# Performance work log

Hardware: AMD Instinct MI355X
Metric: run time of the kernel (lower is better)

Reference implementation:

```python
import jax, jax.numpy as jnp
import numpy as np

N, E, C_IN, C_OUT, K = 50000, 800000, 64, 64, 3

def setup_inputs() -> dict:
    key = jax.random.key(0)
    k1, k2, k3, k4, k5, k6 = jax.random.split(key, 6)
    x = jax.random.normal(k1, (N, C_IN), dtype=jnp.float32)
    row = jax.random.randint(k2, (E,), 0, N)
    col = jax.random.randint(k3, (E,), 0, N)
    # PyG ChebConv removes self loops; avoid generating them
    col = jnp.where(col == row, (col + 1) % N, col)
    edge_index = jnp.stack([row, col])
    edge_weight = jax.random.uniform(k4, (E,), dtype=jnp.float32)
    # ChebConv learned params: one [C_in, C_out] matrix per Chebyshev order, plus bias
    W = jax.random.normal(k5, (K, C_IN, C_OUT), dtype=jnp.float32) / np.sqrt(C_IN).astype(np.float32)
    b = jax.random.normal(k6, (C_OUT,), dtype=jnp.float32) * 0.01
    return {"x": x, "edge_index": edge_index, "edge_weight": edge_weight, "W": W, "b": b}


def reference(x, edge_index, edge_weight, W, b):
    row, col = edge_index[0], edge_index[1]
    # PyG ChebConv.__norm__ with sym normalization and lambda_max = 2.0:
    # L_hat = (2/lambda_max) * (I - D^{-1/2} A D^{-1/2}) - I = -D^{-1/2} A D^{-1/2}
    deg = jax.ops.segment_sum(edge_weight, row, num_segments=N)
    dis = jnp.where(deg > 0, jax.lax.rsqrt(deg), 0.0)  # deg_inv_sqrt, inf -> 0
    w = -dis[row] * edge_weight * dis[col]             # [E] normalized Laplacian weights

    def prop(h):  # sparse matvec: L_hat @ h, [N, C]
        return jax.ops.segment_sum(w[:, None] * h[col], row, num_segments=N)

    # Chebyshev recurrence: T0 = x, T1 = L_hat x, Tk = 2 L_hat T_{k-1} - T_{k-2}
    Tx0 = x
    out = Tx0 @ W[0]
    Tx1 = prop(Tx0)
    out = out + Tx1 @ W[1]
    for k in range(2, K):
        Tx2 = 2.0 * prop(Tx1) - Tx0
        out = out + Tx2 @ W[k]
        Tx0, Tx1 = Tx1, Tx2
    return jax.nn.relu(out + b)
```

## Files before the change

### kernel.cpp

```cpp
#include <hip/hip_runtime.h>
#include <hip/hip_bf16.h>

#define C 64

typedef unsigned short u16;
typedef unsigned int u32;
typedef unsigned long long u64;

__device__ __forceinline__ u16 f2bf_rne(float v) {
    unsigned u = __float_as_uint(v);
    u += 0x7FFFu + ((u >> 16) & 1u);
    return (u16)(u >> 16);
}
__device__ __forceinline__ float bf2f(u16 u) {
    return __uint_as_float((unsigned)u << 16);
}


__global__ __launch_bounds__(256) void p1hist_kernel(const int* __restrict__ row,
                                                     u32* __restrict__ hoff,
                                                     const float* __restrict__ x,
                                                     u16* __restrict__ xh,
                                                     int E, int NB, int total4, int nthreads) {
    __shared__ u32 h[256];
    int t = threadIdx.x;
    int b = blockIdx.x;
    h[t] = 0;
    __syncthreads();
    int base = b * 1024;
#pragma unroll
    for (int u = 0; u < 4; u++) {
        int e = base + u * 256 + t;
        if (e < E) {
            int r = row[e];
            atomicAdd(&h[r >> 8], 1u);
        }
    }
    __syncthreads();
    hoff[(size_t)b * 256 + t] = h[t];

    int gtid = b * 256 + t;
    for (int i = gtid; i < total4; i += nthreads) {
        float4 v = *(const float4*)(x + (size_t)i * 4);
        ushort4 o;
        o.x = f2bf_rne(v.x); o.y = f2bf_rne(v.y);
        o.z = f2bf_rne(v.z); o.w = f2bf_rne(v.w);
        *(ushort4*)(xh + (size_t)i * 4) = o;
    }
}

__global__ __launch_bounds__(256) void scanA_kernel(u32* __restrict__ hoff,
                                                    u32* __restrict__ T, int NB) {
    __shared__ u32 s[256];
    int t = threadIdx.x;
    int d = blockIdx.x;
    u32 carry = 0;
    int nchunk = (NB + 255) / 256;
    for (int ch = 0; ch < nchunk; ch++) {
        int idx = ch * 256 + t;
        u32 v = (idx < NB) ? hoff[(size_t)idx * 256 + d] : 0;
        s[t] = v;
        __syncthreads();
        for (int off = 1; off < 256; off <<= 1) {
            u32 u = (t >= off) ? s[t - off] : 0;
            __syncthreads();
            s[t] += u;
            __syncthreads();
        }
        if (idx < NB) hoff[(size_t)idx * 256 + d] = carry + s[t] - v;
        u32 tot = s[255];
        __syncthreads();
        carry += tot;
    }
    if (t == 0) T[d] = carry;
}

__global__ __launch_bounds__(256) void scanB_kernel(const u32* __restrict__ T,
                                                    u32* __restrict__ Tpre,
                                                    int* __restrict__ rowptr, int N) {
    __shared__ u32 s[256];
    int t = threadIdx.x;
    u32 v = T[t];
    s[t] = v;
    __syncthreads();
    for (int off = 1; off < 256; off <<= 1) {
        u32 u = (t >= off) ? s[t - off] : 0;
        __syncthreads();
        s[t] += u;
        __syncthreads();
    }
    Tpre[t] = s[t] - v;
    if (t == 255) {
        Tpre[256] = s[255];
        rowptr[N] = (int)s[255];
    }
}

__global__ __launch_bounds__(256) void p1scatter_kernel(const int* __restrict__ row,
                                                        const int* __restrict__ col,
                                                        const float* __restrict__ ew,
                                                        const u32* __restrict__ hoff,
                                                        const u32* __restrict__ Tpre,
                                                        u64* __restrict__ pay,
                                                        int E) {
    __shared__ u32 cur[256];
    int t = threadIdx.x;
    int b = blockIdx.x;
    cur[t] = Tpre[t] + hoff[(size_t)b * 256 + t];
    __syncthreads();
    int base = b * 1024;
#pragma unroll
    for (int u = 0; u < 4; u++) {
        int e = base + u * 256 + t;
        if (e < E) {
            u32 r = (u32)row[e];
            u32 c = (u32)col[e];
            u32 rc = (r << 16) | c;
            u32 pos = atomicAdd(&cur[r >> 8], 1u);
            pay[pos] = ((u64)rc << 32) | (u64)__float_as_uint(ew[e]);
        }
    }
}

__global__ __launch_bounds__(256) void p2_kernel(const u64* __restrict__ pay,
                                                 const u32* __restrict__ Tpre,
                                                 int* __restrict__ rowptr,
                                                 float* __restrict__ dis,
                                                 float2* __restrict__ ewc,
                                                 int N) {
    __shared__ u32 h[256];
    __shared__ u32 s[256];
    __shared__ u32 cur[256];
    __shared__ float dsum[256];
    int t = threadIdx.x;
    int bk = blockIdx.x;
    u32 base = Tpre[bk];
    u32 cnt = Tpre[bk + 1] - base;

    h[t] = 0;
    dsum[t] = 0.0f;
    __syncthreads();
    for (u32 j = t; j < cnt; j += 256) {
        u64 v = pay[base + j];
        u32 lr = (u32)(v >> 48) & 255u;
        atomicAdd(&h[lr], 1u);
    }
    __syncthreads();
    u32 hv = h[t];
    s[t] = hv;
    __syncthreads();
    for (int off = 1; off < 256; off <<= 1) {
        u32 u = (t >= off) ? s[t - off] : 0;
        __syncthreads();
        s[t] += u;
        __syncthreads();
    }
    u32 p = s[t] - hv;
    int r = bk * 256 + t;
    if (r < N) rowptr[r] = (int)(base + p);
    cur[t] = base + p;
    __syncthreads();
    for (u32 j = t; j < cnt; j += 256) {
        u64 v = pay[base + j];
        u32 rc = (u32)(v >> 32);
        u32 lr = (rc >> 16) & 255u;
        float w = __uint_as_float((u32)v);
        u32 pos = atomicAdd(&cur[lr], 1u);
        ewc[pos] = make_float2(w, __uint_as_float(rc & 0xffffu));
        atomicAdd(&dsum[lr], w);
    }
    __syncthreads();
    if (r < N) {
        float dv = dsum[t];
        dis[r] = (dv > 0.0f) ? rsqrtf(dv) : 0.0f;
    }
}

template <int NORM>
__global__ __launch_bounds__(256) void spmm2_kernel(
        const int* __restrict__ rowptr,
        float2* __restrict__ ewc,
        const float* __restrict__ dis,
        const u64* __restrict__ h64,
        float* __restrict__ out32,
        u64* __restrict__ outbf,
        int N) {
    __shared__ float2 eds[8][32];

    int tid  = threadIdx.x;
    int hw   = tid >> 5;
    int l32  = tid & 31;
    int e2   = l32 >> 4;
    int cq   = l32 & 15;

    int row = blockIdx.x * 8 + hw;
    if (row >= N) return;

    int beg = rowptr[row];
    int end = rowptr[row + 1];
    float disr = NORM ? dis[row] : 0.0f;

    float a0 = 0.f, a1 = 0.f, a2 = 0.f, a3 = 0.f;

    for (int base = beg; base < end; base += 32) {
        int idx = base + l32;
        bool valid = idx < end;
        float2 ed = valid ? ewc[idx] : make_float2(0.0f, __uint_as_float(0));
        if (NORM) {
            u32 c = __float_as_uint(ed.y);
            float w = -disr * ed.x * dis[c];
            ed = make_float2(w, __uint_as_float(c));
            if (valid) ewc[idx] = ed;
        }
        eds[hw][l32] = ed;
        int cnt = end - base; if (cnt > 32) cnt = 32;
        for (int j = 0; j < cnt; j += 4) {
            float2 f0 = eds[hw][j + e2];
            float2 f1 = eds[hw][j + 2 + e2];
            u32 c0 = __float_as_uint(f0.y);
            u32 c1 = __float_as_uint(f1.y);
            u64 hv0 = h64[(size_t)c0 * 16 + cq];
            u64 hv1 = h64[(size_t)c1 * 16 + cq];
            float w0 = f0.x, w1 = f1.x;
            u32 lo0 = (u32)hv0, hi0 = (u32)(hv0 >> 32);
            u32 lo1 = (u32)hv1, hi1 = (u32)(hv1 >> 32);
            a0 = fmaf(w0, bf2f((u16)(lo0 & 0xffffu)), a0);
            a1 = fmaf(w0, bf2f((u16)(lo0 >> 16)),     a1);
            a2 = fmaf(w0, bf2f((u16)(hi0 & 0xffffu)), a2);
            a3 = fmaf(w0, bf2f((u16)(hi0 >> 16)),     a3);
            a0 = fmaf(w1, bf2f((u16)(lo1 & 0xffffu)), a0);
            a1 = fmaf(w1, bf2f((u16)(lo1 >> 16)),     a1);
            a2 = fmaf(w1, bf2f((u16)(hi1 & 0xffffu)), a2);
            a3 = fmaf(w1, bf2f((u16)(hi1 >> 16)),     a3);
        }
    }

    a0 += __shfl_xor(a0, 16);
    a1 += __shfl_xor(a1, 16);
    a2 += __shfl_xor(a2, 16);
    a3 += __shfl_xor(a3, 16);

    if (e2 == 0) {
        float4 o = make_float4(a0, a1, a2, a3);
        *(float4*)(out32 + (size_t)row * C + 4 * cq) = o;
        u32 p0 = (u32)f2bf_rne(a0) | ((u32)f2bf_rne(a1) << 16);
        u32 p1 = (u32)f2bf_rne(a2) | ((u32)f2bf_rne(a3) << 16);
        outbf[(size_t)row * 16 + cq] = (u64)p0 | ((u64)p1 << 32);
    }
}

__global__ __launch_bounds__(256) void final_gemm_kernel(
        const float* __restrict__ x,
        const float* __restrict__ T1,
        const float* __restrict__ P,
        const float* __restrict__ W,
        const float* __restrict__ b,
        float* __restrict__ out, int N) {
    __shared__ float As[16][64];
    __shared__ float Ws[16][64];

    int t  = threadIdx.x;
    int tx = t & 15;
    int ty = t >> 4;
    int n0 = blockIdx.x * 64;

    int sn = t >> 2;
    int skb = (t & 3) * 4;

    float acc[4][4];
#pragma unroll
    for (int i = 0; i < 4; i++)
#pragma unroll
        for (int j = 0; j < 4; j++) acc[i][j] = 0.0f;

#pragma unroll 1
    for (int s = 0; s < 12; s++) {
        float4 wv = *(const float4*)(W + s * 1024 + t * 4);
        int nn = n0 + sn;
        float4 av = make_float4(0.f, 0.f, 0.f, 0.f);
        if (nn < N) {
            if (s < 4) {
                av = *(const float4*)(x + (size_t)nn * C + s * 16 + skb);
            } else if (s < 8) {
                av = *(const float4*)(T1 + (size_t)nn * C + (s - 4) * 16 + skb);
            } else {
                float4 pv = *(const float4*)(P + (size_t)nn * C + (s - 8) * 16 + skb);
                float4 xv = *(const float4*)(x + (size_t)nn * C + (s - 8) * 16 + skb);
                av = make_float4(2.0f * pv.x - xv.x, 2.0f * pv.y - xv.y,
                                 2.0f * pv.z - xv.z, 2.0f * pv.w - xv.w);
            }
        }
        __syncthreads();
        {
            int wk = (t * 4) >> 6;
            int wc = (t * 4) & 63;
            *(float4*)&Ws[wk][wc] = wv;
        }
        As[skb + 0][sn] = av.x;
        As[skb + 1][sn] = av.y;
        As[skb + 2][sn] = av.z;
        As[skb + 3][sn] = av.w;
        __syncthreads();

#pragma unroll
        for (int kk = 0; kk < 16; kk++) {
            float4 a4 = *(const float4*)&As[kk][ty * 4];
            float4 w4 = *(const float4*)&Ws[kk][tx * 4];
            float ar[4] = {a4.x, a4.y, a4.z, a4.w};
            float wr[4] = {w4.x, w4.y, w4.z, w4.w};
#pragma unroll
            for (int i = 0; i < 4; i++)
#pragma unroll
                for (int j = 0; j < 4; j++)
                    acc[i][j] = fmaf(ar[i], wr[j], acc[i][j]);
        }
    }

    float4 bv = *(const float4*)(b + tx * 4);
    float br[4] = {bv.x, bv.y, bv.z, bv.w};
#pragma unroll
    for (int i = 0; i < 4; i++) {
        int node = n0 + ty * 4 + i;
        if (node < N) {
            float4 o;
            o.x = fmaxf(acc[i][0] + br[0], 0.0f);
            o.y = fmaxf(acc[i][1] + br[1], 0.0f);
            o.z = fmaxf(acc[i][2] + br[2], 0.0f);
            o.w = fmaxf(acc[i][3] + br[3], 0.0f);
            *(float4*)(out + (size_t)node * C + tx * 4) = o;
        }
    }
}

extern "C" void kernel_launch(void* const* d_in, const int* in_sizes, int n_in,
                              void* d_out, int out_size, void* d_ws, size_t ws_size,
                              hipStream_t stream) {
    const float* x  = (const float*)d_in[0];
    const int*   ei = (const int*)d_in[1];
    const float* ew = (const float*)d_in[2];
    const float* W  = (const float*)d_in[3];
    const float* b  = (const float*)d_in[4];
    float* out = (float*)d_out;

    const int N = in_sizes[0] / C;
    const int E = in_sizes[2];
    const int* row = ei;
    const int* col = ei + E;

    char* ws = (char*)d_ws;
    size_t off = 0;
    auto alloc = [&](size_t bytes) {
        void* p = ws + off;
        off = (off + bytes + 255) & ~(size_t)255;
        return p;
    };
    const int NB = (E + 1023) / 1024;
    const int NBUCK = (N + 255) / 256;

    float*  dis    = (float*)alloc((size_t)N * 4);
    int*    rowptr = (int*)alloc((size_t)(N + 1) * 4);
    float2* ewc    = (float2*)alloc((size_t)E * 8);
    u64*    pay    = (u64*)alloc((size_t)E * 8);
    float*  T1     = (float*)alloc((size_t)N * C * 4);
    float*  P      = (float*)alloc((size_t)N * C * 4);
    u32*    hoff   = (u32*)alloc((size_t)NB * 256 * 4);
    u32*    T      = (u32*)alloc((size_t)256 * 4);
    u32*    Tpre   = (u32*)alloc((size_t)257 * 4);
    u16*    xh     = (u16*)alloc((size_t)N * C * 2);
    u16*    T1h    = (u16*)alloc((size_t)N * C * 2);
    u16*    Ph     = (u16*)alloc((size_t)N * C * 2);

    const int B = 256;
    int total4 = N * C / 4;

    p1hist_kernel<<<NB, B, 0, stream>>>(row, hoff, x, xh, E, NB, total4, NB * B);
    scanA_kernel<<<256, B, 0, stream>>>(hoff, T, NB);
    scanB_kernel<<<1, B, 0, stream>>>(T, Tpre, rowptr, N);
    p1scatter_kernel<<<NB, B, 0, stream>>>(row, col, ew, hoff, Tpre, pay, E);
    p2_kernel<<<NBUCK, B, 0, stream>>>(pay, Tpre, rowptr, dis, ewc, N);

    int spmm_blocks = (N + 7) / 8;
    spmm2_kernel<1><<<spmm_blocks, B, 0, stream>>>(rowptr, ewc, dis, (const u64*)xh,
                                                   T1, (u64*)T1h, N);
    spmm2_kernel<0><<<spmm_blocks, B, 0, stream>>>(rowptr, ewc, dis, (const u64*)T1h,
                                                   P, (u64*)Ph, N);

    final_gemm_kernel<<<(N + 63) / 64, B, 0, stream>>>(x, T1, P, W, b, out, N);
}
```

Baseline: 177.1 us.

## Fuse second SpMM into final GEMM, merge scan kernels, recompute edge norms

```diff
diff --git a/kernel.cpp b/kernel.cpp
--- a/kernel.cpp
+++ b/kernel.cpp
@@ -21,10 +21,12 @@
                                                      u32* __restrict__ hoff,
                                                      const float* __restrict__ x,
                                                      u16* __restrict__ xh,
+                                                     u32* __restrict__ done,
                                                      int E, int NB, int total4, int nthreads) {
     __shared__ u32 h[256];
     int t = threadIdx.x;
     int b = blockIdx.x;
+    if (b == 0 && t == 0) *done = 0;
     h[t] = 0;
     __syncthreads();
     int base = b * 1024;
@@ -49,9 +51,14 @@
     }
 }
 
-__global__ __launch_bounds__(256) void scanA_kernel(u32* __restrict__ hoff,
-                                                    u32* __restrict__ T, int NB) {
+__global__ __launch_bounds__(256) void scanAB_kernel(u32* __restrict__ hoff,
+                                                     u32* __restrict__ T,
+                                                     u32* __restrict__ Tpre,
+                                                     int* __restrict__ rowptr,
+                                                     u32* __restrict__ done,
+                                                     int N, int NB) {
     __shared__ u32 s[256];
+    __shared__ u32 lastFlag;
     int t = threadIdx.x;
     int d = blockIdx.x;
     u32 carry = 0;
@@ -73,26 +80,28 @@
         carry += tot;
     }
     if (t == 0) T[d] = carry;
-}
-
-__global__ __launch_bounds__(256) void scanB_kernel(const u32* __restrict__ T,
-                                                    u32* __restrict__ Tpre,
-                                                    int* __restrict__ rowptr, int N) {
-    __shared__ u32 s[256];
-    int t = threadIdx.x;
-    u32 v = T[t];
-    s[t] = v;
-    __syncthreads();
-    for (int off = 1; off < 256; off <<= 1) {
-        u32 u = (t >= off) ? s[t - off] : 0;
-        __syncthreads();
-        s[t] += u;
-        __syncthreads();
-    }
-    Tpre[t] = s[t] - v;
-    if (t == 255) {
-        Tpre[256] = s[255];
-        rowptr[N] = (int)s[255];
+    __threadfence();
+    if (t == 0) {
+        u32 tk = atomicAdd(done, 1u);
+        lastFlag = (tk == 255u) ? 1u : 0u;
+    }
+    __syncthreads();
+    if (lastFlag) {
+        __threadfence();
+        u32 v = T[t];
+        s[t] = v;
+        __syncthreads();
+        for (int off = 1; off < 256; off <<= 1) {
+            u32 u = (t >= off) ? s[t - off] : 0;
+            __syncthreads();
+            s[t] += u;
+            __syncthreads();
+        }
+        Tpre[t] = s[t] - v;
+        if (t == 255) {
+            Tpre[256] = s[255];
+            rowptr[N] = (int)s[255];
+        }
     }
 }
 
@@ -176,10 +185,9 @@
     }
 }
 
-template <int NORM>
-__global__ __launch_bounds__(256) void spmm2_kernel(
+__global__ __launch_bounds__(256) void spmm_t1_kernel(
         const int* __restrict__ rowptr,
-        float2* __restrict__ ewc,
+        const float2* __restrict__ ewc,
         const float* __restrict__ dis,
         const u64* __restrict__ h64,
         float* __restrict__ out32,
@@ -198,7 +206,7 @@
 
     int beg = rowptr[row];
     int end = rowptr[row + 1];
-    float disr = NORM ? dis[row] : 0.0f;
+    float disr = dis[row];
 
     float a0 = 0.f, a1 = 0.f, a2 = 0.f, a3 = 0.f;
 
@@ -206,32 +214,42 @@
         int idx = base + l32;
         bool valid = idx < end;
         float2 ed = valid ? ewc[idx] : make_float2(0.0f, __uint_as_float(0));
-        if (NORM) {
-            u32 c = __float_as_uint(ed.y);
-            float w = -disr * ed.x * dis[c];
-            ed = make_float2(w, __uint_as_float(c));
-            if (valid) ewc[idx] = ed;
-        }
-        eds[hw][l32] = ed;
+        u32 c = __float_as_uint(ed.y);
+        float wv = -disr * ed.x * dis[c];
+        eds[hw][l32] = make_float2(wv, ed.y);
         int cnt = end - base; if (cnt > 32) cnt = 32;
-        for (int j = 0; j < cnt; j += 4) {
+        int cnt8 = (cnt + 7) & ~7;
+        for (int j = 0; j < cnt8; j += 8) {
             float2 f0 = eds[hw][j + e2];
             float2 f1 = eds[hw][j + 2 + e2];
-            u32 c0 = __float_as_uint(f0.y);
-            u32 c1 = __float_as_uint(f1.y);
-            u64 hv0 = h64[(size_t)c0 * 16 + cq];
-            u64 hv1 = h64[(size_t)c1 * 16 + cq];
-            float w0 = f0.x, w1 = f1.x;
-            u32 lo0 = (u32)hv0, hi0 = (u32)(hv0 >> 32);
-            u32 lo1 = (u32)hv1, hi1 = (u32)(hv1 >> 32);
-            a0 = fmaf(w0, bf2f((u16)(lo0 & 0xffffu)), a0);
-            a1 = fmaf(w0, bf2f((u16)(lo0 >> 16)),     a1);
-            a2 = fmaf(w0, bf2f((u16)(hi0 & 0xffffu)), a2);
-            a3 = fmaf(w0, bf2f((u16)(hi0 >> 16)),     a3);
-            a0 = fmaf(w1, bf2f((u16)(lo1 & 0xffffu)), a0);
-            a1 = fmaf(w1, bf2f((u16)(lo1 >> 16)),     a1);
-            a2 = fmaf(w1, bf2f((u16)(hi1 & 0xffffu)), a2);
-            a3 = fmaf(w1, bf2f((u16)(hi1 >> 16)),     a3);
+            float2 f2 = eds[hw][j + 4 + e2];
+            float2 f3 = eds[hw][j + 6 + e2];
+            u64 hv0 = h64[(size_t)__float_as_uint(f0.y) * 16 + cq];
+            u64 hv1 = h64[(size_t)__float_as_uint(f1.y) * 16 + cq];
+            u64 hv2 = h64[(size_t)__float_as_uint(f2.y) * 16 + cq];
+            u64 hv3 = h64[(size_t)__float_as_uint(f3.y) * 16 + cq];
+            float w0 = f0.x, w1 = f1.x, w2 = f2.x, w3 = f3.x;
+            u32 lo, hi;
+            lo = (u32)hv0; hi = (u32)(hv0 >> 32);
+            a0 = fmaf(w0, bf2f((u16)(lo & 0xffffu)), a0);
+            a1 = fmaf(w0, bf2f((u16)(lo >> 16)),     a1);
+            a2 = fmaf(w0, bf2f((u16)(hi & 0xffffu)), a2);
+            a3 = fmaf(w0, bf2f((u16)(hi >> 16)),     a3);
+            lo = (u32)hv1; hi = (u32)(hv1 >> 32);
+            a0 = fmaf(w1, bf2f((u16)(lo & 0xffffu)), a0);
+            a1 = fmaf(w1, bf2f((u16)(lo >> 16)),     a1);
+            a2 = fmaf(w1, bf2f((u16)(hi & 0xffffu)), a2);
+            a3 = fmaf(w1, bf2f((u16)(hi >> 16)),     a3);
+            lo = (u32)hv2; hi = (u32)(hv2 >> 32);
+            a0 = fmaf(w2, bf2f((u16)(lo & 0xffffu)), a0);
+            a1 = fmaf(w2, bf2f((u16)(lo >> 16)),     a1);
+            a2 = fmaf(w2, bf2f((u16)(hi & 0xffffu)), a2);
+            a3 = fmaf(w2, bf2f((u16)(hi >> 16)),     a3);
+            lo = (u32)hv3; hi = (u32)(hv3 >> 32);
+            a0 = fmaf(w3, bf2f((u16)(lo & 0xffffu)), a0);
+            a1 = fmaf(w3, bf2f((u16)(lo >> 16)),     a1);
+            a2 = fmaf(w3, bf2f((u16)(hi & 0xffffu)), a2);
+            a3 = fmaf(w3, bf2f((u16)(hi >> 16)),     a3);
         }
     }
 
@@ -241,29 +259,89 @@
     a3 += __shfl_xor(a3, 16);
 
     if (e2 == 0) {
-        float4 o = make_float4(a0, a1, a2, a3);
-        *(float4*)(out32 + (size_t)row * C + 4 * cq) = o;
+        *(float4*)(out32 + (size_t)row * C + 4 * cq) = make_float4(a0, a1, a2, a3);
         u32 p0 = (u32)f2bf_rne(a0) | ((u32)f2bf_rne(a1) << 16);
         u32 p1 = (u32)f2bf_rne(a2) | ((u32)f2bf_rne(a3) << 16);
         outbf[(size_t)row * 16 + cq] = (u64)p0 | ((u64)p1 << 32);
     }
 }
 
-__global__ __launch_bounds__(256) void final_gemm_kernel(
+__global__ __launch_bounds__(256) void spmm_gemm_kernel(
+        const int* __restrict__ rowptr,
+        const float2* __restrict__ ewc,
+        const float* __restrict__ dis,
+        const u64* __restrict__ t1h,
         const float* __restrict__ x,
         const float* __restrict__ T1,
-        const float* __restrict__ P,
         const float* __restrict__ W,
         const float* __restrict__ b,
         float* __restrict__ out, int N) {
+    __shared__ float T2s[64][68];
     __shared__ float As[16][64];
     __shared__ float Ws[16][64];
+    __shared__ float2 eds[16][16];
 
     int t  = threadIdx.x;
+    int q  = t >> 4;
+    int cq = t & 15;
+    int n0 = blockIdx.x * 64;
+
+    for (int rr = 0; rr < 4; rr++) {
+        int row = n0 + q * 4 + rr;
+        if (row < N) {
+            int beg = rowptr[row];
+            int end = rowptr[row + 1];
+            float disr = dis[row];
+            float a0 = 0.f, a1 = 0.f, a2 = 0.f, a3 = 0.f;
+            for (int base = beg; base < end; base += 16) {
+                int idx = base + cq;
+                float2 ed = (idx < end) ? ewc[idx] : make_float2(0.0f, __uint_as_float(0));
+                u32 c = __float_as_uint(ed.y);
+                float wv = -disr * ed.x * dis[c];
+                eds[q][cq] = make_float2(wv, ed.y);
+                int cnt = end - base; if (cnt > 16) cnt = 16;
+                int cnt4 = (cnt + 3) & ~3;
+                for (int j = 0; j < cnt4; j += 4) {
+                    float2 f0 = eds[q][j];
+                    float2 f1 = eds[q][j + 1];
+                    float2 f2 = eds[q][j + 2];
+                    float2 f3 = eds[q][j + 3];
+                    u64 h0 = t1h[(size_t)__float_as_uint(f0.y) * 16 + cq];
+                    u64 h1 = t1h[(size_t)__float_as_uint(f1.y) * 16 + cq];
+                    u64 h2 = t1h[(size_t)__float_as_uint(f2.y) * 16 + cq];
+                    u64 h3 = t1h[(size_t)__float_as_uint(f3.y) * 16 + cq];
+                    u32 lo, hi;
+                    lo = (u32)h0; hi = (u32)(h0 >> 32);
+                    a0 = fmaf(f0.x, bf2f((u16)(lo & 0xffffu)), a0);
+                    a1 = fmaf(f0.x, bf2f((u16)(lo >> 16)),     a1);
+                    a2 = fmaf(f0.x, bf2f((u16)(hi & 0xffffu)), a2);
+                    a3 = fmaf(f0.x, bf2f((u16)(hi >> 16)),     a3);
+                    lo = (u32)h1; hi = (u32)(h1 >> 32);
+                    a0 = fmaf(f1.x, bf2f((u16)(lo & 0xffffu)), a0);
+                    a1 = fmaf(f1.x, bf2f((u16)(lo >> 16)),     a1);
+                    a2 = fmaf(f1.x, bf2f((u16)(hi & 0xffffu)), a2);
+                    a3 = fmaf(f1.x, bf2f((u16)(hi >> 16)),     a3);
+                    lo = (u32)h2; hi = (u32)(h2 >> 32);
+                    a0 = fmaf(f2.x, bf2f((u16)(lo & 0xffffu)), a0);
+                    a1 = fmaf(f2.x, bf2f((u16)(lo >> 16)),     a1);
+                    a2 = fmaf(f2.x, bf2f((u16)(hi & 0xffffu)), a2);
+                    a3 = fmaf(f2.x, bf2f((u16)(hi >> 16)),     a3);
+                    lo = (u32)h3; hi = (u32)(h3 >> 32);
+                    a0 = fmaf(f3.x, bf2f((u16)(lo & 0xffffu)), a0);
+                    a1 = fmaf(f3.x, bf2f((u16)(lo >> 16)),     a1);
+                    a2 = fmaf(f3.x, bf2f((u16)(hi & 0xffffu)), a2);
+                    a3 = fmaf(f3.x, bf2f((u16)(hi >> 16)),     a3);
+                }
+            }
+            float4 xv = *(const float4*)(x + (size_t)row * C + 4 * cq);
+            *(float4*)&T2s[q * 4 + rr][4 * cq] =
+                make_float4(2.f * a0 - xv.x, 2.f * a1 - xv.y,
+                            2.f * a2 - xv.z, 2.f * a3 - xv.w);
+        }
+    }
+
     int tx = t & 15;
     int ty = t >> 4;
-    int n0 = blockIdx.x * 64;
-
     int sn = t >> 2;
     int skb = (t & 3) * 4;
 
@@ -276,19 +354,11 @@
 #pragma unroll 1
     for (int s = 0; s < 12; s++) {
         float4 wv = *(const float4*)(W + s * 1024 + t * 4);
+        float4 av = make_float4(0.f, 0.f, 0.f, 0.f);
         int nn = n0 + sn;
-        float4 av = make_float4(0.f, 0.f, 0.f, 0.f);
-        if (nn < N) {
-            if (s < 4) {
-                av = *(const float4*)(x + (size_t)nn * C + s * 16 + skb);
-            } else if (s < 8) {
-                av = *(const float4*)(T1 + (size_t)nn * C + (s - 4) * 16 + skb);
-            } else {
-                float4 pv = *(const float4*)(P + (size_t)nn * C + (s - 8) * 16 + skb);
-                float4 xv = *(const float4*)(x + (size_t)nn * C + (s - 8) * 16 + skb);
-                av = make_float4(2.0f * pv.x - xv.x, 2.0f * pv.y - xv.y,
-                                 2.0f * pv.z - xv.z, 2.0f * pv.w - xv.w);
-            }
+        if (s < 8 && nn < N) {
+            const float* src = (s < 4) ? x : T1;
+            av = *(const float4*)(src + (size_t)nn * C + (s & 3) * 16 + skb);
         }
         __syncthreads();
         {
@@ -296,23 +366,42 @@
             int wc = (t * 4) & 63;
             *(float4*)&Ws[wk][wc] = wv;
         }
-        As[skb + 0][sn] = av.x;
-        As[skb + 1][sn] = av.y;
-        As[skb + 2][sn] = av.z;
-        As[skb + 3][sn] = av.w;
-        __syncthreads();
-
-#pragma unroll
-        for (int kk = 0; kk < 16; kk++) {
-            float4 a4 = *(const float4*)&As[kk][ty * 4];
-            float4 w4 = *(const float4*)&Ws[kk][tx * 4];
-            float ar[4] = {a4.x, a4.y, a4.z, a4.w};
-            float wr[4] = {w4.x, w4.y, w4.z, w4.w};
-#pragma unroll
-            for (int i = 0; i < 4; i++)
-#pragma unroll
-                for (int j = 0; j < 4; j++)
-                    acc[i][j] = fmaf(ar[i], wr[j], acc[i][j]);
+        if (s < 8) {
+            As[skb + 0][sn] = av.x;
+            As[skb + 1][sn] = av.y;
+            As[skb + 2][sn] = av.z;
+            As[skb + 3][sn] = av.w;
+        }
+        __syncthreads();
+
+        if (s < 8) {
+#pragma unroll
+            for (int kk = 0; kk < 16; kk++) {
+                float4 a4 = *(const float4*)&As[kk][ty * 4];
+                float4 w4 = *(const float4*)&Ws[kk][tx * 4];
+                float ar[4] = {a4.x, a4.y, a4.z, a4.w};
+                float wr[4] = {w4.x, w4.y, w4.z, w4.w};
+#pragma unroll
+                for (int i = 0; i < 4; i++)
+#pragma unroll
+                    for (int j = 0; j < 4; j++)
+                        acc[i][j] = fmaf(ar[i], wr[j], acc[i][j]);
+            }
+        } else {
+            int ks = (s - 8) * 16;
+#pragma unroll
+            for (int kk = 0; kk < 16; kk++) {
+                float4 w4 = *(const float4*)&Ws[kk][tx * 4];
+                float wr[4] = {w4.x, w4.y, w4.z, w4.w};
+                float ar[4];
+#pragma unroll
+                for (int i = 0; i < 4; i++) ar[i] = T2s[ty * 4 + i][ks + kk];
+#pragma unroll
+                for (int i = 0; i < 4; i++)
+#pragma unroll
+                    for (int j = 0; j < 4; j++)
+                        acc[i][j] = fmaf(ar[i], wr[j], acc[i][j]);
+            }
         }
     }
 
@@ -362,28 +451,24 @@
     float2* ewc    = (float2*)alloc((size_t)E * 8);
     u64*    pay    = (u64*)alloc((size_t)E * 8);
     float*  T1     = (float*)alloc((size_t)N * C * 4);
-    float*  P      = (float*)alloc((size_t)N * C * 4);
     u32*    hoff   = (u32*)alloc((size_t)NB * 256 * 4);
     u32*    T      = (u32*)alloc((size_t)256 * 4);
     u32*    Tpre   = (u32*)alloc((size_t)257 * 4);
+    u32*    done   = (u32*)alloc((size_t)256);
     u16*    xh     = (u16*)alloc((size_t)N * C * 2);
     u16*    T1h    = (u16*)alloc((size_t)N * C * 2);
-    u16*    Ph     = (u16*)alloc((size_t)N * C * 2);
 
     const int B = 256;
     int total4 = N * C / 4;
 
-    p1hist_kernel<<<NB, B, 0, stream>>>(row, hoff, x, xh, E, NB, total4, NB * B);
-    scanA_kernel<<<256, B, 0, stream>>>(hoff, T, NB);
-    scanB_kernel<<<1, B, 0, stream>>>(T, Tpre, rowptr, N);
+    p1hist_kernel<<<NB, B, 0, stream>>>(row, hoff, x, xh, done, E, NB, total4, NB * B);
+    scanAB_kernel<<<256, B, 0, stream>>>(hoff, T, Tpre, rowptr, done, N, NB);
     p1scatter_kernel<<<NB, B, 0, stream>>>(row, col, ew, hoff, Tpre, pay, E);
     p2_kernel<<<NBUCK, B, 0, stream>>>(pay, Tpre, rowptr, dis, ewc, N);
 
     int spmm_blocks = (N + 7) / 8;
-    spmm2_kernel<1><<<spmm_blocks, B, 0, stream>>>(rowptr, ewc, dis, (const u64*)xh,
-                                                   T1, (u64*)T1h, N);
-    spmm2_kernel<0><<<spmm_blocks, B, 0, stream>>>(rowptr, ewc, dis, (const u64*)T1h,
-                                                   P, (u64*)Ph, N);
-
-    final_gemm_kernel<<<(N + 63) / 64, B, 0, stream>>>(x, T1, P, W, b, out, N);
-}
+    spmm_t1_kernel<<<spmm_blocks, B, 0, stream>>>(rowptr, ewc, dis, (const u64*)xh,
+                                                  T1, (u64*)T1h, N);
+    spmm_gemm_kernel<<<(N + 63) / 64, B, 0, stream>>>(rowptr, ewc, dis, (const u64*)T1h,
+                                                      x, T1, W, b, out, N);
+}
```

New measurement: 208.3 us. 17.6% more time.

## Fuse scan kernels, recompute edge weights in both SpMMs, unroll gather loop

Applied to the files above, without the earlier changes.

```diff
diff --git a/kernel.cpp b/kernel.cpp
--- a/kernel.cpp
+++ b/kernel.cpp
@@ -21,10 +21,12 @@
                                                      u32* __restrict__ hoff,
                                                      const float* __restrict__ x,
                                                      u16* __restrict__ xh,
+                                                     u32* __restrict__ done,
                                                      int E, int NB, int total4, int nthreads) {
     __shared__ u32 h[256];
     int t = threadIdx.x;
     int b = blockIdx.x;
+    if (b == 0 && t == 0) *done = 0;
     h[t] = 0;
     __syncthreads();
     int base = b * 1024;
@@ -49,9 +51,14 @@
     }
 }
 
-__global__ __launch_bounds__(256) void scanA_kernel(u32* __restrict__ hoff,
-                                                    u32* __restrict__ T, int NB) {
+__global__ __launch_bounds__(256) void scanAB_kernel(u32* __restrict__ hoff,
+                                                     u32* __restrict__ T,
+                                                     u32* __restrict__ Tpre,
+                                                     int* __restrict__ rowptr,
+                                                     u32* __restrict__ done,
+                                                     int N, int NB) {
     __shared__ u32 s[256];
+    __shared__ u32 lastFlag;
     int t = threadIdx.x;
     int d = blockIdx.x;
     u32 carry = 0;
@@ -73,26 +80,28 @@
         carry += tot;
     }
     if (t == 0) T[d] = carry;
-}
-
-__global__ __launch_bounds__(256) void scanB_kernel(const u32* __restrict__ T,
-                                                    u32* __restrict__ Tpre,
-                                                    int* __restrict__ rowptr, int N) {
-    __shared__ u32 s[256];
-    int t = threadIdx.x;
-    u32 v = T[t];
-    s[t] = v;
-    __syncthreads();
-    for (int off = 1; off < 256; off <<= 1) {
-        u32 u = (t >= off) ? s[t - off] : 0;
-        __syncthreads();
-        s[t] += u;
-        __syncthreads();
-    }
-    Tpre[t] = s[t] - v;
-    if (t == 255) {
-        Tpre[256] = s[255];
-        rowptr[N] = (int)s[255];
+    __threadfence();
+    if (t == 0) {
+        u32 tk = atomicAdd(done, 1u);
+        lastFlag = (tk == 255u) ? 1u : 0u;
+    }
+    __syncthreads();
+    if (lastFlag) {
+        __threadfence();
+        u32 v = T[t];
+        s[t] = v;
+        __syncthreads();
+        for (int off = 1; off < 256; off <<= 1) {
+            u32 u = (t >= off) ? s[t - off] : 0;
+            __syncthreads();
+            s[t] += u;
+            __syncthreads();
+        }
+        Tpre[t] = s[t] - v;
+        if (t == 255) {
+            Tpre[256] = s[255];
+            rowptr[N] = (int)s[255];
+        }
     }
 }
 
@@ -176,10 +185,10 @@
     }
 }
 
-template <int NORM>
-__global__ __launch_bounds__(256) void spmm2_kernel(
+template <int WBF>
+__global__ __launch_bounds__(256) void spmm_kernel(
         const int* __restrict__ rowptr,
-        float2* __restrict__ ewc,
+        const float2* __restrict__ ewc,
         const float* __restrict__ dis,
         const u64* __restrict__ h64,
         float* __restrict__ out32,
@@ -198,7 +207,7 @@
 
     int beg = rowptr[row];
     int end = rowptr[row + 1];
-    float disr = NORM ? dis[row] : 0.0f;
+    float disr = dis[row];
 
     float a0 = 0.f, a1 = 0.f, a2 = 0.f, a3 = 0.f;
 
@@ -206,32 +215,42 @@
         int idx = base + l32;
         bool valid = idx < end;
         float2 ed = valid ? ewc[idx] : make_float2(0.0f, __uint_as_float(0));
-        if (NORM) {
-            u32 c = __float_as_uint(ed.y);
-            float w = -disr * ed.x * dis[c];
-            ed = make_float2(w, __uint_as_float(c));
-            if (valid) ewc[idx] = ed;
-        }
-        eds[hw][l32] = ed;
+        u32 c = __float_as_uint(ed.y);
+        float wv = -disr * ed.x * dis[c];
+        eds[hw][l32] = make_float2(wv, ed.y);
         int cnt = end - base; if (cnt > 32) cnt = 32;
-        for (int j = 0; j < cnt; j += 4) {
+        int cnt8 = (cnt + 7) & ~7;
+        for (int j = 0; j < cnt8; j += 8) {
             float2 f0 = eds[hw][j + e2];
             float2 f1 = eds[hw][j + 2 + e2];
-            u32 c0 = __float_as_uint(f0.y);
-            u32 c1 = __float_as_uint(f1.y);
-            u64 hv0 = h64[(size_t)c0 * 16 + cq];
-            u64 hv1 = h64[(size_t)c1 * 16 + cq];
-            float w0 = f0.x, w1 = f1.x;
-            u32 lo0 = (u32)hv0, hi0 = (u32)(hv0 >> 32);
-            u32 lo1 = (u32)hv1, hi1 = (u32)(hv1 >> 32);
-            a0 = fmaf(w0, bf2f((u16)(lo0 & 0xffffu)), a0);
-            a1 = fmaf(w0, bf2f((u16)(lo0 >> 16)),     a1);
-            a2 = fmaf(w0, bf2f((u16)(hi0 & 0xffffu)), a2);
-            a3 = fmaf(w0, bf2f((u16)(hi0 >> 16)),     a3);
-            a0 = fmaf(w1, bf2f((u16)(lo1 & 0xffffu)), a0);
-            a1 = fmaf(w1, bf2f((u16)(lo1 >> 16)),     a1);
-            a2 = fmaf(w1, bf2f((u16)(hi1 & 0xffffu)), a2);
-            a3 = fmaf(w1, bf2f((u16)(hi1 >> 16)),     a3);
+            float2 f2 = eds[hw][j + 4 + e2];
+            float2 f3 = eds[hw][j + 6 + e2];
+            u64 hv0 = h64[(size_t)__float_as_uint(f0.y) * 16 + cq];
+            u64 hv1 = h64[(size_t)__float_as_uint(f1.y) * 16 + cq];
+            u64 hv2 = h64[(size_t)__float_as_uint(f2.y) * 16 + cq];
+            u64 hv3 = h64[(size_t)__float_as_uint(f3.y) * 16 + cq];
+            float w0 = f0.x, w1 = f1.x, w2 = f2.x, w3 = f3.x;
+            u32 lo, hi;
+            lo = (u32)hv0; hi = (u32)(hv0 >> 32);
+            a0 = fmaf(w0, bf2f((u16)(lo & 0xffffu)), a0);
+            a1 = fmaf(w0, bf2f((u16)(lo >> 16)),     a1);
+            a2 = fmaf(w0, bf2f((u16)(hi & 0xffffu)), a2);
+            a3 = fmaf(w0, bf2f((u16)(hi >> 16)),     a3);
+            lo = (u32)hv1; hi = (u32)(hv1 >> 32);
+            a0 = fmaf(w1, bf2f((u16)(lo & 0xffffu)), a0);
+            a1 = fmaf(w1, bf2f((u16)(lo >> 16)),     a1);
+            a2 = fmaf(w1, bf2f((u16)(hi & 0xffffu)), a2);
+            a3 = fmaf(w1, bf2f((u16)(hi >> 16)),     a3);
+            lo = (u32)hv2; hi = (u32)(hv2 >> 32);
+            a0 = fmaf(w2, bf2f((u16)(lo & 0xffffu)), a0);
+            a1 = fmaf(w2, bf2f((u16)(lo >> 16)),     a1);
+            a2 = fmaf(w2, bf2f((u16)(hi & 0xffffu)), a2);
+            a3 = fmaf(w2, bf2f((u16)(hi >> 16)),     a3);
+            lo = (u32)hv3; hi = (u32)(hv3 >> 32);
+            a0 = fmaf(w3, bf2f((u16)(lo & 0xffffu)), a0);
+            a1 = fmaf(w3, bf2f((u16)(lo >> 16)),     a1);
+            a2 = fmaf(w3, bf2f((u16)(hi & 0xffffu)), a2);
+            a3 = fmaf(w3, bf2f((u16)(hi >> 16)),     a3);
         }
     }
 
@@ -241,11 +260,12 @@
     a3 += __shfl_xor(a3, 16);
 
     if (e2 == 0) {
-        float4 o = make_float4(a0, a1, a2, a3);
-        *(float4*)(out32 + (size_t)row * C + 4 * cq) = o;
-        u32 p0 = (u32)f2bf_rne(a0) | ((u32)f2bf_rne(a1) << 16);
-        u32 p1 = (u32)f2bf_rne(a2) | ((u32)f2bf_rne(a3) << 16);
-        outbf[(size_t)row * 16 + cq] = (u64)p0 | ((u64)p1 << 32);
+        *(float4*)(out32 + (size_t)row * C + 4 * cq) = make_float4(a0, a1, a2, a3);
+        if (WBF) {
+            u32 p0 = (u32)f2bf_rne(a0) | ((u32)f2bf_rne(a1) << 16);
+            u32 p1 = (u32)f2bf_rne(a2) | ((u32)f2bf_rne(a3) << 16);
+            outbf[(size_t)row * 16 + cq] = (u64)p0 | ((u64)p1 << 32);
+        }
     }
 }
 
@@ -366,24 +386,23 @@
     u32*    hoff   = (u32*)alloc((size_t)NB * 256 * 4);
     u32*    T      = (u32*)alloc((size_t)256 * 4);
     u32*    Tpre   = (u32*)alloc((size_t)257 * 4);
+    u32*    done   = (u32*)alloc((size_t)256);
     u16*    xh     = (u16*)alloc((size_t)N * C * 2);
     u16*    T1h    = (u16*)alloc((size_t)N * C * 2);
-    u16*    Ph     = (u16*)alloc((size_t)N * C * 2);
 
     const int B = 256;
     int total4 = N * C / 4;
 
-    p1hist_kernel<<<NB, B, 0, stream>>>(row, hoff, x, xh, E, NB, total4, NB * B);
-    scanA_kernel<<<256, B, 0, stream>>>(hoff, T, NB);
-    scanB_kernel<<<1, B, 0, stream>>>(T, Tpre, rowptr, N);
+    p1hist_kernel<<<NB, B, 0, stream>>>(row, hoff, x, xh, done, E, NB, total4, NB * B);
+    scanAB_kernel<<<256, B, 0, stream>>>(hoff, T, Tpre, rowptr, done, N, NB);
     p1scatter_kernel<<<NB, B, 0, stream>>>(row, col, ew, hoff, Tpre, pay, E);
     p2_kernel<<<NBUCK, B, 0, stream>>>(pay, Tpre, rowptr, dis, ewc, N);
 
     int spmm_blocks = (N + 7) / 8;
-    spmm2_kernel<1><<<spmm_blocks, B, 0, stream>>>(rowptr, ewc, dis, (const u64*)xh,
-                                                   T1, (u64*)T1h, N);
-    spmm2_kernel<0><<<spmm_blocks, B, 0, stream>>>(rowptr, ewc, dis, (const u64*)T1h,
-                                                   P, (u64*)Ph, N);
+    spmm_kernel<1><<<spmm_blocks, B, 0, stream>>>(rowptr, ewc, dis, (const u64*)xh,
+                                                  T1, (u64*)T1h, N);
+    spmm_kernel<0><<<spmm_blocks, B, 0, stream>>>(rowptr, ewc, dis, (const u64*)T1h,
+                                                  P, (u64*)nullptr, N);
 
     final_gemm_kernel<<<(N + 63) / 64, B, 0, stream>>>(x, T1, P, W, b, out, N);
 }
```

Result: slower. 190.0 us (+7.3%).
